# Optimization experiments

Hardware: AMD Instinct MI355X
Metric: run time of the kernel (lower is better)

## Reference

```python
import jax, jax.numpy as jnp
import numpy as np

SIGMA_D = 0.2
SIGMA_A = 15.0
FACTOR_A = 180.0 / (SIGMA_A * np.pi)
HIDDEN = 256


def sinusoidal_embedding(x, d_model):
    # GeoTransformer-style: interleaved sin/cos pairs along last dim.
    div_term = jnp.exp(jnp.arange(0, d_model, 2, dtype=x.dtype) * (-np.log(10000.0) / d_model))  # (d/2,)
    omegas = x[..., None] * div_term  # (..., d/2)
    emb = jnp.stack([jnp.sin(omegas), jnp.cos(omegas)], axis=-1)  # (..., d/2, 2)
    return emb.reshape(*x.shape, d_model)


def _indices(points, anchor_points):
    # pairwise sq dist: |p|^2 + |a|^2 - 2 p.a, clamped at 0
    sq = (jnp.sum(points ** 2, -1)[:, :, None]
          + jnp.sum(anchor_points ** 2, -1)[:, None, :]
          - 2.0 * jnp.einsum('bnd,bkd->bnk', points, anchor_points))
    dist_map = jnp.sqrt(jnp.maximum(sq, 0.0))  # (B,N,K)
    d_indices = dist_map / SIGMA_D
    ref_vectors = points[:, :, None, :] - anchor_points[:, None, :, :]  # (B,N,K,3)
    # gather with indices [1,2,...,K-1,0] == roll by -1 along K
    anc_vectors = jnp.roll(ref_vectors, shift=-1, axis=2)
    sin_values = jnp.linalg.norm(jnp.cross(ref_vectors, anc_vectors, axis=-1), axis=-1)
    cos_values = jnp.sum(ref_vectors * anc_vectors, axis=-1)
    angles = jnp.arctan2(sin_values, cos_values)
    a_indices = angles * FACTOR_A
    return d_indices, a_indices


def setup_inputs() -> dict:
    key = jax.random.key(0)
    ks = jax.random.split(key, 5)
    B, N, K, H = 1, 4096, 64, HIDDEN
    return {
        'points': jax.random.normal(ks[0], (B, N, 3), jnp.float32),
        'anchor_points': jax.random.normal(ks[1], (B, K, 3), jnp.float32),
        'cor_score': jax.random.uniform(ks[2], (K,), jnp.float32),
        'Wa': jax.random.normal(ks[3], (H, H), jnp.float32) * (1.0 / np.sqrt(H)),
        'ba': jnp.zeros((H,), jnp.float32),
        'Wd': jax.random.normal(ks[4], (H, H), jnp.float32) * (1.0 / np.sqrt(H)),
        'bd': jnp.zeros((H,), jnp.float32),
    }


def reference(points, anchor_points, cor_score, Wa, ba, Wd, bd):
    d_idx, a_idx = _indices(points, anchor_points)  # computed under no_grad in torch
    d_idx = jax.lax.stop_gradient(d_idx)
    a_idx = jax.lax.stop_gradient(a_idx)
    a_emb = sinusoidal_embedding(a_idx, HIDDEN)          # (B,N,K,H)
    a_emb = jnp.einsum('bnkh,oh->bnko', a_emb, Wa) + ba
    d_emb = sinusoidal_embedding(d_idx, HIDDEN)
    d_emb = jnp.einsum('bnkh,oh->bnko', d_emb, Wd) + bd
    # reduction_a == 'max'
    d_emb = jnp.max(d_emb, axis=2)
    a_emb = jnp.max(a_emb, axis=2)
    return d_emb + a_emb  # (B,N,H)
```

## Files before the change

### kernel.cpp

```cpp
#include <hip/hip_runtime.h>
#include <hip/hip_bf16.h>
#include <math.h>


typedef __attribute__((ext_vector_type(8))) short short8;
typedef __attribute__((ext_vector_type(16))) float f32x16;
typedef __attribute__((ext_vector_type(4))) unsigned int uint4v;
typedef __attribute__((ext_vector_type(4))) float float4v;
typedef __attribute__((ext_vector_type(4))) unsigned short ushort4v;

#define HH 256
#define KK 112
#define P_PTS 4
#define NPTS 4096

__device__ __forceinline__ unsigned short f2bf(float f) {
    union { float f; unsigned int u; } v; v.f = f;
    unsigned int r = v.u + 0x7fffu + ((v.u >> 16) & 1u);
    return (unsigned short)(r >> 16);
}

__device__ __forceinline__ unsigned int pack_sc(float s, float c) {
    union { __hip_bfloat162 h; unsigned int u; } v;
    v.h = __float22bfloat162_rn(make_float2(s, c));
    return v.u;
}

__global__ __launch_bounds__(64)
void prep_w_kernel(const float* __restrict__ Wa, const float* __restrict__ Wd,
                   unsigned short* __restrict__ wbf) {
    const int r = blockIdx.x * 64 + threadIdx.x;
    const int t = r >> 8, o = r & 255;
    const float* W = (t == 0 ? Wd : Wa) + o * HH;
    unsigned short* dst = wbf + (t * HH + o) * KK;
    #pragma unroll
    for (int e4 = 0; e4 < 26; ++e4) {
        const float4v w4 = *(const float4v*)(W + e4 * 4);
        ushort4v s4;
        #pragma unroll
        for (int j = 0; j < 4; ++j) s4[j] = f2bf(w4[j]);
        *(ushort4v*)(dst + e4 * 4) = s4;
    }
    float u1 = 0.f, u2 = 0.f, u3 = 0.f, u4 = 0.f, v = 0.f;
    float d = 0.023713737056616554f;
    for (int i = 52; i < 128; ++i) {
        const float d2 = d * d;
        const float ws = W[2 * i], wc = W[2 * i + 1];
        u1 += d * ws;
        u3 += -(d * d2) * (1.0f / 6.0f) * ws;
        u2 += -0.5f * d2 * wc;
        u4 += (d2 * d2) * (1.0f / 24.0f) * wc;
        v  += wc;
        d *= 0.9305720409297085f;
    }
    dst[104] = f2bf(u1);
    dst[105] = f2bf(u2);
    dst[106] = f2bf(u3);
    dst[107] = f2bf(u4);
    dst[108] = f2bf(v);
    dst[109] = 0; dst[110] = 0; dst[111] = 0;
}


__global__ __launch_bounds__(512, 8)
void cgse_main(const float* __restrict__ points,
               const float* __restrict__ anchors,
               const unsigned short* __restrict__ wbf,
               const float* __restrict__ ba,
               const float* __restrict__ bd,
               float* __restrict__ out) {
    __shared__ __align__(16) unsigned short E[2][64 * 128];
    __shared__ float xs[2][P_PTS][64];
    __shared__ float anch[192];

    const int tid = threadIdx.x;
    const int wave = tid >> 6, lane = tid & 63;
    const int l5 = lane & 31, half = lane >> 5;
    const int base = blockIdx.x * P_PTS;
    const int col = wave * 32 + l5;

    if (tid < 192) anch[tid] = anchors[tid];
    __syncthreads();
    if (wave < 4) {
        const int k2 = (lane + 1) & 63;
        const int pn = base + wave;
        const float px = points[pn * 3 + 0], py = points[pn * 3 + 1], pz = points[pn * 3 + 2];
        const float r1x = px - anch[lane * 3 + 0];
        const float r1y = py - anch[lane * 3 + 1];
        const float r1z = pz - anch[lane * 3 + 2];
        const float r2x = px - anch[k2 * 3 + 0];
        const float r2y = py - anch[k2 * 3 + 1];
        const float r2z = pz - anch[k2 * 3 + 2];
        xs[0][wave][lane] = sqrtf(r1x * r1x + r1y * r1y + r1z * r1z) * 5.0f;
        const float cx = r1y * r2z - r1z * r2y;
        const float cy = r1z * r2x - r1x * r2z;
        const float cz = r1x * r2y - r1y * r2x;
        const float sv = sqrtf(cx * cx + cy * cy + cz * cz);
        const float cv = r1x * r2x + r1y * r2y + r1z * r2z;
        xs[1][wave][lane] = atan2f(sv, cv) * 3.8197186342054885f;
    }

    const float bias = ba[col] + bd[col];

    const float cw = 0.15915494309189535f * __expf(-(float)wave * 0.2878231366242554f);

    const int wbase = (lane << 8) ^ (((lane & 7) ^ wave) << 4);
    const int rbase = (l5 << 8) ^ ((l5 & 7) << 4) ^ (half << 4);

    auto fill_chunk = [&](char* eb, int c, float x, float xc) {
        uint4v w;
        if (wave == 5 && c == 1) {
            const float x2 = x * x;
            w[0] = pack_sc(x, x2);
            w[1] = pack_sc(x2 * x, x2 * x2);
            w[2] = pack_sc(1.0f, 0.0f);
            w[3] = 0u;
        } else {
            const float t0 = c ? xc * 0.1f : xc;
            const float t[4] = {t0, t0 * 0.9305720409297085f,
                                t0 * 0.8659643233600653f, t0 * 0.8058421877614819f};
            #pragma unroll
            for (int j = 0; j < 4; ++j)
                w[j] = pack_sc(__builtin_amdgcn_sinf(t[j]), __builtin_amdgcn_cosf(t[j]));
        }
        *(uint4v*)(eb + (wbase ^ (c << 7))) = w;
    };

    short8 bw[7];
    auto loadW = [&](int t) {
        const unsigned short* wr = wbf + (t * HH + col) * KK + half * 8;
        #pragma unroll
        for (int ks = 0; ks < 7; ++ks)
            bw[ks] = *(const short8*)(wr + ks * 16);
    };

    auto htree = [&](const f32x16& a) -> float {
        const float v0 = fmaxf(fmaxf(a[0], a[1]), a[2]);
        const float v1 = fmaxf(fmaxf(a[3], a[4]), a[5]);
        const float v2 = fmaxf(fmaxf(a[6], a[7]), a[8]);
        const float v3 = fmaxf(fmaxf(a[9], a[10]), a[11]);
        const float v4 = fmaxf(fmaxf(a[12], a[13]), a[14]);
        const float w0 = fmaxf(fmaxf(v0, v1), v2);
        const float w1 = fmaxf(fmaxf(v3, v4), a[15]);
        return fmaxf(w0, w1);
    };

    loadW(0);
    __syncthreads();
    {
        const float x = xs[0][0][lane], xc = x * cw;
        fill_chunk((char*)E[0], 0, x, xc);
        if (wave < 6) fill_chunk((char*)E[0], 1, x, xc);
    }

    float dm[P_PTS];

    #pragma unroll
    for (int q = 0; q < 4; ++q) {
        __syncthreads();
        const char* ebC = (const char*)E[q & 1];
        char* ebN = (char*)E[(q & 1) ^ 1];
        {
            const float xn = (q < 3) ? xs[0][q + 1][lane] : xs[1][0][lane];
            const float xcn = xn * cw;
            fill_chunk(ebN, 0, xn, xcn);
            if (wave < 6) fill_chunk(ebN, 1, xn, xcn);
        }

        float mh[2];
        #pragma unroll
        for (int hh = 0; hh < 2; ++hh) {
            f32x16 acc;
            #pragma unroll
            for (int r = 0; r < 16; ++r) acc[r] = 0.f;
            #pragma unroll
            for (int ks = 0; ks < 7; ++ks) {
                const short8 afr = *(const short8*)
                    (ebC + ((rbase ^ (ks << 5)) + hh * 8192));
                __builtin_amdgcn_s_setprio(1);
                acc = __builtin_amdgcn_mfma_f32_32x32x16_bf16(afr, bw[ks], acc, 0, 0, 0);
                __builtin_amdgcn_s_setprio(0);
            }
            mh[hh] = htree(acc);
        }
        float m = fmaxf(mh[0], mh[1]);
        m = fmaxf(m, __shfl_down(m, 32));
        dm[q] = m;
    }

    loadW(1);

    #pragma unroll
    for (int q = 0; q < 4; ++q) {
        __syncthreads();
        const char* ebC = (const char*)E[q & 1];
        char* ebN = (char*)E[(q & 1) ^ 1];
        if (q < 3) {
            const float xn = xs[1][q + 1][lane];
            const float xcn = xn * cw;
            fill_chunk(ebN, 0, xn, xcn);
            if (wave < 6) fill_chunk(ebN, 1, xn, xcn);
        }

        float mh[2];
        #pragma unroll
        for (int hh = 0; hh < 2; ++hh) {
            f32x16 acc;
            #pragma unroll
            for (int r = 0; r < 16; ++r) acc[r] = 0.f;
            #pragma unroll
            for (int ks = 0; ks < 7; ++ks) {
                const short8 afr = *(const short8*)
                    (ebC + ((rbase ^ (ks << 5)) + hh * 8192));
                __builtin_amdgcn_s_setprio(1);
                acc = __builtin_amdgcn_mfma_f32_32x32x16_bf16(afr, bw[ks], acc, 0, 0, 0);
                __builtin_amdgcn_s_setprio(0);
            }
            mh[hh] = htree(acc);
        }
        float m = fmaxf(mh[0], mh[1]);
        m = fmaxf(m, __shfl_down(m, 32));
        if (lane < 32)
            out[(base + q) * HH + col] = m + dm[q] + bias;
    }
}

extern "C" void kernel_launch(void* const* d_in, const int* in_sizes, int n_in,
                              void* d_out, int out_size, void* d_ws, size_t ws_size,
                              hipStream_t stream) {
    const float* points  = (const float*)d_in[0];
    const float* anchors = (const float*)d_in[1];
    const float* Wa = (const float*)d_in[3];
    const float* ba = (const float*)d_in[4];
    const float* Wd = (const float*)d_in[5];
    const float* bd = (const float*)d_in[6];

    unsigned short* wbf = (unsigned short*)d_ws;

    hipLaunchKernelGGL(prep_w_kernel, dim3(8), dim3(64), 0, stream, Wa, Wd, wbf);
    hipLaunchKernelGGL(cgse_main, dim3(NPTS / P_PTS), dim3(512), 0, stream,
                       points, anchors, wbf, ba, bd, (float*)d_out);
}
```

Baseline: 101.2 us.

## Give each wave 64 output columns and process two points per block step

Each block now handles 8 points, in two groups of four waves. Each wave computes two 32-column output tiles that share one LDS A-fragment per MFMA pair, so LDS reads per MFMA are halved. The embedding tile is repacked into four frequency chunks per wave, with new scale factors. The E buffer is doubled, which doubles LDS use per block and raises register pressure (launch bounds hint drops to 4), trading occupancy and block count for operand reuse. A stray dead load was left in the fill routine.

```diff
diff --git a/kernel.cpp b/kernel.cpp
--- a/kernel.cpp
+++ b/kernel.cpp
@@ -11,7 +11,7 @@
 
 #define HH 256
 #define KK 112
-#define P_PTS 4
+#define P_PTS 8
 #define NPTS 4096
 
 __device__ __forceinline__ unsigned short f2bf(float f) {
@@ -62,14 +62,14 @@
 }
 
 
-__global__ __launch_bounds__(512, 8)
+__global__ __launch_bounds__(512, 4)
 void cgse_main(const float* __restrict__ points,
                const float* __restrict__ anchors,
                const unsigned short* __restrict__ wbf,
                const float* __restrict__ ba,
                const float* __restrict__ bd,
                float* __restrict__ out) {
-    __shared__ __align__(16) unsigned short E[2][64 * 128];
+    __shared__ __align__(16) unsigned short E[2][2][64 * 128];
     __shared__ float xs[2][P_PTS][64];
     __shared__ float anch[192];
 
@@ -77,11 +77,12 @@
     const int wave = tid >> 6, lane = tid & 63;
     const int l5 = lane & 31, half = lane >> 5;
     const int base = blockIdx.x * P_PTS;
-    const int col = wave * 32 + l5;
+    const int pg = wave >> 2;
+    const int w4 = wave & 3;
 
     if (tid < 192) anch[tid] = anchors[tid];
     __syncthreads();
-    if (wave < 4) {
+    {
         const int k2 = (lane + 1) & 63;
         const int pn = base + wave;
         const float px = points[pn * 3 + 0], py = points[pn * 3 + 1], pz = points[pn * 3 + 2];
@@ -100,38 +101,59 @@
         xs[1][wave][lane] = atan2f(sv, cv) * 3.8197186342054885f;
     }
 
-    const float bias = ba[col] + bd[col];
-
-    const float cw = 0.15915494309189535f * __expf(-(float)wave * 0.2878231366242554f);
-
-    const int wbase = (lane << 8) ^ (((lane & 7) ^ wave) << 4);
+    float bias[2];
+    #pragma unroll
+    for (int ntp = 0; ntp < 2; ++ntp) {
+        const int c = w4 * 64 + ntp * 32 + l5;
+        bias[ntp] = ba[c] + bd[c];
+    }
+
+    const float cw = 0.15915494309189535f * __expf(-(float)w4 * 0.2878231366242554f);
+
+    const int tb = pg * 16384;
+    const int wbase = (lane << 8) ^ (((lane & 7) ^ w4) << 4);
     const int rbase = (l5 << 8) ^ ((l5 & 7) << 4) ^ (half << 4);
 
     auto fill_chunk = [&](char* eb, int c, float x, float xc) {
         uint4v w;
-        if (wave == 5 && c == 1) {
+        if (w4 == 1 && c == 3) {
             const float x2 = x * x;
             w[0] = pack_sc(x, x2);
             w[1] = pack_sc(x2 * x, x2 * x2);
             w[2] = pack_sc(1.0f, 0.0f);
             w[3] = 0u;
         } else {
-            const float t0 = c ? xc * 0.1f : xc;
+            const float DCI[4] = {1.0f, 0.31622776601683794f, 0.1f,
+                                  0.03162277660168379f};
+            const float t0 = xc * DCI[c];
             const float t[4] = {t0, t0 * 0.9305720409297085f,
                                 t0 * 0.8659643233600653f, t0 * 0.8058421877614819f};
             #pragma unroll
             for (int j = 0; j < 4; ++j)
                 w[j] = pack_sc(__builtin_amdgcn_sinf(t[j]), __builtin_amdgcn_cosf(t[j]));
         }
-        *(uint4v*)(eb + (wbase ^ (c << 7))) = w;
-    };
-
-    short8 bw[7];
+        *(uint4v*)(eb + (wbase ^ (c << 6)));
+        *(uint4v*)(eb + (wbase ^ (c << 6))) = w;
+    };
+
+    auto fill_tile = [&](char* eb, float x) {
+        const float xc = x * cw;
+        fill_chunk(eb, 0, x, xc);
+        fill_chunk(eb, 1, x, xc);
+        fill_chunk(eb, 2, x, xc);
+        if (w4 < 2) fill_chunk(eb, 3, x, xc);
+    };
+
+    short8 bw[2][7];
     auto loadW = [&](int t) {
-        const unsigned short* wr = wbf + (t * HH + col) * KK + half * 8;
-        #pragma unroll
-        for (int ks = 0; ks < 7; ++ks)
-            bw[ks] = *(const short8*)(wr + ks * 16);
+        #pragma unroll
+        for (int ntp = 0; ntp < 2; ++ntp) {
+            const unsigned short* wr =
+                wbf + (t * HH + w4 * 64 + ntp * 32 + l5) * KK + half * 8;
+            #pragma unroll
+            for (int ks = 0; ks < 7; ++ks)
+                bw[ntp][ks] = *(const short8*)(wr + ks * 16);
+        }
     };
 
     auto htree = [&](const f32x16& a) -> float {
@@ -147,45 +169,45 @@
 
     loadW(0);
     __syncthreads();
-    {
-        const float x = xs[0][0][lane], xc = x * cw;
-        fill_chunk((char*)E[0], 0, x, xc);
-        if (wave < 6) fill_chunk((char*)E[0], 1, x, xc);
-    }
-
-    float dm[P_PTS];
+    fill_tile((char*)E[0][pg], xs[0][pg][lane]);
+
+    float dm[4][2];
 
     #pragma unroll
     for (int q = 0; q < 4; ++q) {
         __syncthreads();
-        const char* ebC = (const char*)E[q & 1];
-        char* ebN = (char*)E[(q & 1) ^ 1];
-        {
-            const float xn = (q < 3) ? xs[0][q + 1][lane] : xs[1][0][lane];
-            const float xcn = xn * cw;
-            fill_chunk(ebN, 0, xn, xcn);
-            if (wave < 6) fill_chunk(ebN, 1, xn, xcn);
-        }
-
-        float mh[2];
+        const char* ebC = (const char*)E[q & 1][pg];
+        char* ebN = (char*)E[(q & 1) ^ 1][pg];
+        fill_tile(ebN, (q < 3) ? xs[0][2 * (q + 1) + pg][lane] : xs[1][pg][lane]);
+
+        float m[2];
         #pragma unroll
         for (int hh = 0; hh < 2; ++hh) {
-            f32x16 acc;
-            #pragma unroll
-            for (int r = 0; r < 16; ++r) acc[r] = 0.f;
+            f32x16 acc[2];
+            #pragma unroll
+            for (int ntp = 0; ntp < 2; ++ntp)
+                #pragma unroll
+                for (int r = 0; r < 16; ++r) acc[ntp][r] = 0.f;
             #pragma unroll
             for (int ks = 0; ks < 7; ++ks) {
                 const short8 afr = *(const short8*)
                     (ebC + ((rbase ^ (ks << 5)) + hh * 8192));
                 __builtin_amdgcn_s_setprio(1);
-                acc = __builtin_amdgcn_mfma_f32_32x32x16_bf16(afr, bw[ks], acc, 0, 0, 0);
+                acc[0] = __builtin_amdgcn_mfma_f32_32x32x16_bf16(afr, bw[0][ks], acc[0], 0, 0, 0);
+                acc[1] = __builtin_amdgcn_mfma_f32_32x32x16_bf16(afr, bw[1][ks], acc[1], 0, 0, 0);
                 __builtin_amdgcn_s_setprio(0);
             }
-            mh[hh] = htree(acc);
-        }
-        float m = fmaxf(mh[0], mh[1]);
-        m = fmaxf(m, __shfl_down(m, 32));
-        dm[q] = m;
+            #pragma unroll
+            for (int ntp = 0; ntp < 2; ++ntp) {
+                const float h = htree(acc[ntp]);
+                m[ntp] = hh ? fmaxf(m[ntp], h) : h;
+            }
+        }
+        #pragma unroll
+        for (int ntp = 0; ntp < 2; ++ntp) {
+            m[ntp] = fmaxf(m[ntp], __shfl_down(m[ntp], 32));
+            dm[q][ntp] = m[ntp];
+        }
     }
 
     loadW(1);
@@ -193,35 +215,40 @@
     #pragma unroll
     for (int q = 0; q < 4; ++q) {
         __syncthreads();
-        const char* ebC = (const char*)E[q & 1];
-        char* ebN = (char*)E[(q & 1) ^ 1];
-        if (q < 3) {
-            const float xn = xs[1][q + 1][lane];
-            const float xcn = xn * cw;
-            fill_chunk(ebN, 0, xn, xcn);
-            if (wave < 6) fill_chunk(ebN, 1, xn, xcn);
-        }
-
-        float mh[2];
+        const char* ebC = (const char*)E[q & 1][pg];
+        char* ebN = (char*)E[(q & 1) ^ 1][pg];
+        if (q < 3) fill_tile(ebN, xs[1][2 * (q + 1) + pg][lane]);
+
+        float m[2];
         #pragma unroll
         for (int hh = 0; hh < 2; ++hh) {
-            f32x16 acc;
-            #pragma unroll
-            for (int r = 0; r < 16; ++r) acc[r] = 0.f;
+            f32x16 acc[2];
+            #pragma unroll
+            for (int ntp = 0; ntp < 2; ++ntp)
+                #pragma unroll
+                for (int r = 0; r < 16; ++r) acc[ntp][r] = 0.f;
             #pragma unroll
             for (int ks = 0; ks < 7; ++ks) {
                 const short8 afr = *(const short8*)
                     (ebC + ((rbase ^ (ks << 5)) + hh * 8192));
                 __builtin_amdgcn_s_setprio(1);
-                acc = __builtin_amdgcn_mfma_f32_32x32x16_bf16(afr, bw[ks], acc, 0, 0, 0);
+                acc[0] = __builtin_amdgcn_mfma_f32_32x32x16_bf16(afr, bw[0][ks], acc[0], 0, 0, 0);
+                acc[1] = __builtin_amdgcn_mfma_f32_32x32x16_bf16(afr, bw[1][ks], acc[1], 0, 0, 0);
                 __builtin_amdgcn_s_setprio(0);
             }
-            mh[hh] = htree(acc);
-        }
-        float m = fmaxf(mh[0], mh[1]);
-        m = fmaxf(m, __shfl_down(m, 32));
-        if (lane < 32)
-            out[(base + q) * HH + col] = m + dm[q] + bias;
+            #pragma unroll
+            for (int ntp = 0; ntp < 2; ++ntp) {
+                const float h = htree(acc[ntp]);
+                m[ntp] = hh ? fmaxf(m[ntp], h) : h;
+            }
+        }
+        #pragma unroll
+        for (int ntp = 0; ntp < 2; ++ntp) {
+            m[ntp] = fmaxf(m[ntp], __shfl_down(m[ntp], 32));
+            if (lane < 32)
+                out[(base + 2 * q + pg) * HH + w4 * 64 + ntp * 32 + l5]
+                    = m[ntp] + dm[q][ntp] + bias[ntp];
+        }
     }
 }
 
```

Result: slower. 103.3 us (+2.1%).
